# Kernel tuning notes

Measured on AMD Instinct MI355X. Metric: run time of the kernel, lower is better.

The kernel has to match this reference:

```python
import jax, jax.numpy as jnp
import numpy as np


def _sobel_mag(x_bchw):
    # per-channel Sobel gradient magnitude, then mean over channels -> [B,1,H,W]
    B, C, H, W = x_bchw.shape
    kx = jnp.array([[-1, 0, 1], [-2, 0, 2], [-1, 0, 1]], dtype=x_bchw.dtype).reshape(1, 1, 3, 3)
    ky = jnp.array([[-1, -2, -1], [0, 0, 0], [1, 2, 1]], dtype=x_bchw.dtype).reshape(1, 1, 3, 3)
    xf = x_bchw.reshape(B * C, 1, H, W)
    dn = ('NCHW', 'OIHW', 'NCHW')
    gx = jax.lax.conv_general_dilated(xf, kx, (1, 1), 'SAME', dimension_numbers=dn)
    gy = jax.lax.conv_general_dilated(xf, ky, (1, 1), 'SAME', dimension_numbers=dn)
    mag = jnp.sqrt(gx * gx + gy * gy + 1e-8).reshape(B, C, H, W)
    return mag.mean(axis=1, keepdims=True)


def _bi_wkv(w, u, k, v):
    # Bidirectional WKV (Vision-RWKV):
    # y_t = (sum_{i!=t} exp(k_i - (|t-i|-1)*w) v_i + exp(u+k_t) v_t)
    #     / (sum_{i!=t} exp(k_i - (|t-i|-1)*w)     + exp(u+k_t))
    # w,u: [C];  k,v: [B,T,C]. Numerically stable prefix scans in both directions.
    B, T, C = k.shape
    kt = jnp.transpose(k, (1, 0, 2))  # [T,B,C]
    vt = jnp.transpose(v, (1, 0, 2))

    def scan_dir(ks, vs):
        def step(carry, kv):
            a, b, pp = carry  # running num, den at log-offset pp (exclusive prefix)
            kk, vv = kv
            out = (a, b, pp)
            ww = pp - w  # decay one step
            p = jnp.maximum(ww, kk)
            e1 = jnp.exp(ww - p)
            e2 = jnp.exp(kk - p)
            return (e1 * a + e2 * vv, e1 * b + e2, p), out
        init = (jnp.zeros((B, C), k.dtype), jnp.zeros((B, C), k.dtype),
                jnp.full((B, C), -1e38, k.dtype))
        _, (a, b, pp) = jax.lax.scan(step, init, (ks, vs))
        return a, b, pp

    af, bf, pf = scan_dir(kt, vt)                       # contributions i < t
    ab, bb, pb = scan_dir(kt[::-1], vt[::-1])           # contributions i > t
    ab, bb, pb = ab[::-1], bb[::-1], pb[::-1]

    ps = u + kt                                         # self term exponent
    m = jnp.maximum(jnp.maximum(pf, pb), ps)
    ef = jnp.exp(pf - m)
    eb = jnp.exp(pb - m)
    es = jnp.exp(ps - m)
    num = af * ef + ab * eb + es * vt
    den = bf * ef + bb * eb + es
    return jnp.transpose(num / den, (1, 0, 2))  # [B,T,C]


def setup_inputs() -> dict:
    key = jax.random.key(0)
    ks = jax.random.split(key, 8)
    B, H, W, C = 8, 64, 64, 256
    T = H * W
    s = 1.0 / np.sqrt(C)
    return {
        'x': jax.random.normal(ks[0], (B, T, C), jnp.float32),
        'Wk': jax.random.normal(ks[1], (C, C), jnp.float32) * s,
        'Wv': jax.random.normal(ks[2], (C, C), jnp.float32) * s,
        'Wr': jax.random.normal(ks[3], (C, C), jnp.float32) * s,
        'Wo': jax.random.normal(ks[4], (C, C), jnp.float32) * s,
        'spatial_decay': jax.random.uniform(ks[5], (C,), jnp.float32, 0.5, 1.5),
        'spatial_first': jax.random.uniform(ks[6], (C,), jnp.float32, 0.5, 1.5),
        'H': H,
        'W': W,
    }


def reference(x, Wk, Wv, Wr, Wo, spatial_decay, spatial_first, H, W):
    B, T, C = x.shape
    k = x @ Wk.T
    v = x @ Wv.T
    r = x @ Wr.T
    sr = jax.nn.sigmoid(r)
    # edge gate
    x_hw = jnp.transpose(x, (0, 2, 1)).reshape(B, C, H, W)
    edge_g = jax.nn.sigmoid(_sobel_mag(x_hw)).reshape(B, 1, T)
    sr = sr + jnp.transpose(edge_g, (0, 2, 1))
    # bi-directional WKV with w,u scaled by 1/T (as in forward)
    xwkv = _bi_wkv(spatial_decay / T, spatial_first / T, k, v)
    return (sr * xwkv) @ Wo.T
```

## Files before the change

### kernel.cpp

```cpp
#include <hip/hip_runtime.h>
#include <hip/hip_bf16.h>

#define TB 8
#define TT 4096
#define TC 256
#define NC2 128
#define CL2 32

#define K2 512
#define BM 128
#define BN 128
#define BK 32

typedef _Float16 half8 __attribute__((ext_vector_type(8)));
typedef _Float16 half2v __attribute__((ext_vector_type(2)));
typedef float floatx4 __attribute__((ext_vector_type(4)));

#define GLDS16(g, l) __builtin_amdgcn_global_load_lds( \
    (const __attribute__((address_space(1))) void*)(g), \
    (__attribute__((address_space(3))) void*)(l), 16, 0, 0)

__global__ __launch_bounds__(256) void convert_x(
    const float* __restrict__ x, _Float16* __restrict__ X2, int n4)
{
    int t = blockIdx.x * 256 + threadIdx.x;
    if (t >= n4) return;
    float4 xv = ((const float4*)x)[t];
    half8 o;
    o[0] = (_Float16)xv.x; o[1] = (_Float16)(xv.x - (float)o[0]);
    o[2] = (_Float16)xv.y; o[3] = (_Float16)(xv.y - (float)o[2]);
    o[4] = (_Float16)xv.z; o[5] = (_Float16)(xv.z - (float)o[4]);
    o[6] = (_Float16)xv.w; o[7] = (_Float16)(xv.w - (float)o[6]);
    ((half8*)X2)[t] = o;
}

__global__ __launch_bounds__(256) void convert_w(
    const float* __restrict__ Wk, const float* __restrict__ Wv,
    const float* __restrict__ Wr, const float* __restrict__ Wo,
    _Float16* __restrict__ W2, _Float16* __restrict__ Wo2)
{
    int t = blockIdx.x * 256 + threadIdx.x;
    int wsel = t >> 16;
    int i = t & 65535;
    const float* src = (wsel == 0) ? Wk : (wsel == 1) ? Wv : (wsel == 2) ? Wr : Wo;
    _Float16* dst = (wsel < 3) ? (W2 + (size_t)wsel * TC * K2) : Wo2;
    _Float16 h = (_Float16)src[i];
    half2v p; p.x = h; p.y = h;
    *(half2v*)(dst + 2 * (size_t)i) = p;
}

__global__ __launch_bounds__(256) void gemm_f16(
    const _Float16* __restrict__ A2,
    const _Float16* __restrict__ W0, const _Float16* __restrict__ W1,
    const _Float16* __restrict__ W2p,
    float* __restrict__ C0, float* __restrict__ C1, float* __restrict__ C2,
    int sigmoid_mask)
{
    __shared__ _Float16 As[BM * BK];
    __shared__ _Float16 Bs[BN * BK];

    int by = blockIdx.y;
    int wsel = by >> 1;
    const _Float16* W = (wsel == 0) ? W0 : (wsel == 1) ? W1 : W2p;
    float* Cc         = (wsel == 0) ? C0 : (wsel == 1) ? C1 : C2;
    int col0 = (by & 1) * BN;
    int row0 = blockIdx.x * BM;
    int sig = (sigmoid_mask >> wsel) & 1;

    int tid = threadIdx.x;
    int lane = tid & 63;
    int wv = tid >> 6;
    int qm = (wv >> 1) * 64;
    int qn = (wv & 1) * 64;
    int mrow = lane & 15;
    int kgrp = (lane >> 4) * 8;

    const _Float16* Ag = A2 + (size_t)row0 * K2;
    const _Float16* Bg = W + (size_t)col0 * K2;

    floatx4 acc[4][4];
    #pragma unroll
    for (int i = 0; i < 4; i++)
        #pragma unroll
        for (int j = 0; j < 4; j++)
            acc[i][j] = (floatx4){0.f, 0.f, 0.f, 0.f};

    for (int kb = 0; kb < K2; kb += BK) {
        __syncthreads();
        #pragma unroll
        for (int r = 0; r < 2; r++) {
            int seg = r * 256 + tid;
            int row = seg >> 2;
            int ks = (seg & 3) * 8;
            GLDS16(Ag + (size_t)row * K2 + kb + ks, &As[seg * 8]);
            GLDS16(Bg + (size_t)row * K2 + kb + ks, &Bs[seg * 8]);
        }
        __syncthreads();
        half8 a[4], b[4];
        #pragma unroll
        for (int i = 0; i < 4; i++)
            a[i] = *(const half8*)&As[(qm + i * 16 + mrow) * BK + kgrp];
        #pragma unroll
        for (int j = 0; j < 4; j++)
            b[j] = *(const half8*)&Bs[(qn + j * 16 + mrow) * BK + kgrp];
        #pragma unroll
        for (int i = 0; i < 4; i++)
            #pragma unroll
            for (int j = 0; j < 4; j++)
                acc[i][j] = __builtin_amdgcn_mfma_f32_16x16x32_f16(
                    a[i], b[j], acc[i][j], 0, 0, 0);
    }

    int mr0 = (lane >> 4) * 4;
    int nc = lane & 15;
    #pragma unroll
    for (int i = 0; i < 4; i++) {
        #pragma unroll
        for (int r = 0; r < 4; r++) {
            int m = row0 + qm + i * 16 + mr0 + r;
            float* crow = Cc + (size_t)m * TC + col0 + qn;
            #pragma unroll
            for (int j = 0; j < 4; j++) {
                float vvv = acc[i][j][r];
                if (sig) vvv = 1.f / (1.f + __expf(-vvv));
                crow[j * 16 + nc] = vvv;
            }
        }
    }
}

__global__ __launch_bounds__(256) void sobel_edge(
    const float* __restrict__ x, float* __restrict__ edge)
{
    int t = blockIdx.x & (TT - 1);
    int b = blockIdx.x >> 12;
    int h = t >> 6, w = t & 63;
    int c = threadIdx.x;

    float n[3][3];
    #pragma unroll
    for (int dh = 0; dh < 3; dh++) {
        int hh = h + dh - 1;
        #pragma unroll
        for (int dw = 0; dw < 3; dw++) {
            int ww = w + dw - 1;
            float val = 0.f;
            if (hh >= 0 && hh < 64 && ww >= 0 && ww < 64)
                val = x[((size_t)(b * TT + (hh << 6) + ww)) * TC + c];
            n[dh][dw] = val;
        }
    }
    float gx = (n[0][2] - n[0][0]) + 2.f * (n[1][2] - n[1][0]) + (n[2][2] - n[2][0]);
    float gy = (n[2][0] + 2.f * n[2][1] + n[2][2]) - (n[0][0] + 2.f * n[0][1] + n[0][2]);
    float mag = sqrtf(gx * gx + gy * gy + 1e-8f);

    #pragma unroll
    for (int off = 32; off > 0; off >>= 1) mag += __shfl_down(mag, off, 64);
    __shared__ float part[4];
    if ((threadIdx.x & 63) == 0) part[threadIdx.x >> 6] = mag;
    __syncthreads();
    if (threadIdx.x == 0) {
        float s = part[0] + part[1] + part[2] + part[3];
        edge[blockIdx.x] = 1.f / (1.f + __expf(-s * (1.f / 256.f)));
    }
}

__global__ __launch_bounds__(256) void wkv_chunk_sums(
    const float* __restrict__ kp, const float* __restrict__ vp,
    const float* __restrict__ decay,
    float* __restrict__ SaF, float* __restrict__ SbF,
    float* __restrict__ RaB, float* __restrict__ RbB)
{
    int tid = blockIdx.x * 256 + threadIdx.x;
    int c = tid & 255;
    int j = (tid >> 8) & (NC2 - 1);
    int b = tid >> 15;
    float w = decay[c] * (1.f / (float)TT);
    float d = __expf(-w);
    size_t base = ((size_t)(b * TT + j * CL2)) * TC + c;
    float Sa = 0.f, Sb = 0.f, Ra = 0.f, Rb = 0.f, pw = 1.f;
    #pragma unroll
    for (int i = 0; i < CL2; i++) {
        float kk = kp[base + (size_t)i * TC];
        float vv = vp[base + (size_t)i * TC];
        float ek = __expf(kk);
        float ekv = ek * vv;
        Sa = fmaf(d, Sa, ekv);
        Sb = fmaf(d, Sb, ek);
        Ra = fmaf(pw, ekv, Ra);
        Rb = fmaf(pw, ek, Rb);
        pw *= d;
    }
    int idx = (b * NC2 + j) * TC + c;
    SaF[idx] = Sa; SbF[idx] = Sb; RaB[idx] = Ra; RbB[idx] = Rb;
}

__global__ __launch_bounds__(256) void wkv_carries(
    const float* __restrict__ SaF, const float* __restrict__ SbF,
    const float* __restrict__ RaB, const float* __restrict__ RbB,
    const float* __restrict__ decay,
    float* __restrict__ CfA, float* __restrict__ CfB,
    float* __restrict__ CbA, float* __restrict__ CbB)
{
    int tid = blockIdx.x * 256 + threadIdx.x;
    int c = tid & 255;
    int b = tid >> 8;
    float w = decay[c] * (1.f / (float)TT);
    float D = __expf(-(float)CL2 * w);
    float cfa = 0.f, cfb = 0.f;
    for (int j = 0; j < NC2; j++) {
        int idx = (b * NC2 + j) * TC + c;
        CfA[idx] = cfa; CfB[idx] = cfb;
        cfa = fmaf(D, cfa, SaF[idx]);
        cfb = fmaf(D, cfb, SbF[idx]);
    }
    float cba = 0.f, cbb = 0.f;
    for (int j = NC2 - 1; j >= 0; j--) {
        int idx = (b * NC2 + j) * TC + c;
        CbA[idx] = cba; CbB[idx] = cbb;
        cba = fmaf(D, cba, RaB[idx]);
        cbb = fmaf(D, cbb, RbB[idx]);
    }
}

__global__ __launch_bounds__(256) void wkv_combine(
    const float* __restrict__ kp, const float* __restrict__ vp,
    const float* __restrict__ srp, const float* __restrict__ edgep,
    const float* __restrict__ decay, const float* __restrict__ first,
    const float* __restrict__ CfA, const float* __restrict__ CfB,
    const float* __restrict__ CbA, const float* __restrict__ CbB,
    _Float16* __restrict__ Y2)
{
    int bid = blockIdx.x;
    int j = bid & (NC2 - 1);
    int b = bid >> 7;
    int c = threadIdx.x;

    float w = decay[c] * (1.f / (float)TT);
    float d = __expf(-w);
    float eu = __expf(first[c] * (1.f / (float)TT));
    int cidx = (b * NC2 + j) * TC + c;
    size_t base = ((size_t)(b * TT + j * CL2)) * TC + c;

    float abArr[CL2], bbArr[CL2];
    float ab = CbA[cidx], bb = CbB[cidx];
    #pragma unroll
    for (int i = CL2 - 1; i >= 0; i--) {
        float kk = kp[base + (size_t)i * TC];
        float vv = vp[base + (size_t)i * TC];
        float ek = __expf(kk);
        abArr[i] = ab; bbArr[i] = bb;
        ab = fmaf(d, ab, ek * vv);
        bb = fmaf(d, bb, ek);
    }
    float af = CfA[cidx], bf = CfB[cidx];
    #pragma unroll
    for (int i = 0; i < CL2; i++) {
        size_t idx = base + (size_t)i * TC;
        float kk = kp[idx];
        float vv = vp[idx];
        float srv = srp[idx];
        float ek = __expf(kk);
        float es = ek * eu;
        float num = af + abArr[i] + es * vv;
        float den = bf + bbArr[i] + es;
        float ev = edgep[b * TT + j * CL2 + i];
        float yv = (srv + ev) * (num / den);
        _Float16 yh = (_Float16)yv;
        _Float16 yl = (_Float16)(yv - (float)yh);
        half2v p; p.x = yh; p.y = yl;
        size_t m = (size_t)(b * TT + j * CL2 + i);
        *(half2v*)(Y2 + m * K2 + 2 * c) = p;
        af = fmaf(d, af, ek * vv);
        bf = fmaf(d, bf, ek);
    }
}

extern "C" void kernel_launch(void* const* d_in, const int* in_sizes, int n_in,
                              void* d_out, int out_size, void* d_ws, size_t ws_size,
                              hipStream_t stream)
{
    const float* x      = (const float*)d_in[0];
    const float* Wk     = (const float*)d_in[1];
    const float* Wv     = (const float*)d_in[2];
    const float* Wr     = (const float*)d_in[3];
    const float* Wo     = (const float*)d_in[4];
    const float* sdecay = (const float*)d_in[5];
    const float* sfirst = (const float*)d_in[6];
    float* out = (float*)d_out;

    char* ws = (char*)d_ws;
    size_t off = 0;
    const size_t MB32 = (size_t)TB * TT * TC * sizeof(float);
    const size_t XH   = (size_t)TB * TT * K2 * sizeof(_Float16);
    _Float16* X2  = (_Float16*)(ws + off); off += XH;
    float* kbuf  = (float*)(ws + off); off += MB32;
    float* vbuf  = (float*)(ws + off); off += MB32;
    float* srbuf = (float*)(ws + off); off += MB32;
    _Float16* W2  = (_Float16*)(ws + off); off += (size_t)3 * TC * K2 * sizeof(_Float16);
    _Float16* Wo2 = (_Float16*)(ws + off); off += (size_t)TC * K2 * sizeof(_Float16);
    float* edge  = (float*)(ws + off); off += (size_t)TB * TT * sizeof(float);
    const size_t CHB = (size_t)TB * NC2 * TC * sizeof(float);
    float* SaF = (float*)(ws + off); off += CHB;
    float* SbF = (float*)(ws + off); off += CHB;
    float* RaB = (float*)(ws + off); off += CHB;
    float* RbB = (float*)(ws + off); off += CHB;
    float* CfA = (float*)(ws + off); off += CHB;
    float* CfB = (float*)(ws + off); off += CHB;
    float* CbA = (float*)(ws + off); off += CHB;
    float* CbB = (float*)(ws + off); off += CHB;

    const int MBLK = (TB * TT) / BM;
    const int n4 = TB * TT * TC / 4;

    convert_w<<<(4 * TC * TC) / 256, 256, 0, stream>>>(Wk, Wv, Wr, Wo, W2, Wo2);
    convert_x<<<(n4 + 255) / 256, 256, 0, stream>>>(x, X2, n4);
    sobel_edge<<<TB * TT, 256, 0, stream>>>(x, edge);

    gemm_f16<<<dim3(MBLK, 6), 256, 0, stream>>>(
        X2, W2, W2 + (size_t)TC * K2, W2 + (size_t)2 * TC * K2,
        kbuf, vbuf, srbuf, 4);

    wkv_chunk_sums<<<(TB * NC2 * TC) / 256, 256, 0, stream>>>(
        kbuf, vbuf, sdecay, SaF, SbF, RaB, RbB);
    wkv_carries<<<(TB * TC) / 256, 256, 0, stream>>>(
        SaF, SbF, RaB, RbB, sdecay, CfA, CfB, CbA, CbB);
    wkv_combine<<<TB * NC2, 256, 0, stream>>>(
        kbuf, vbuf, srbuf, edge, sdecay, sfirst, CfA, CfB, CbA, CbB, X2);

    gemm_f16<<<dim3(MBLK, 2), 256, 0, stream>>>(
        X2, Wo2, Wo2, Wo2, out, out, out, 0);
}
```

Baseline: 247.6 us.

## Fuse x conversion into Sobel, store exp(k) as fp16, parallelize carries, widen GEMM K-tile

The x fp16 split-conversion is folded into the Sobel edge kernel, which removes one full pass over x. The k projection GEMM now applies exp in its epilogue and writes fp16 through a swizzled LDS tile, so later WKV kernels read half the bytes and skip their exp calls. The GEMM K tile grows to 64 with an XOR-swizzled LDS layout to reduce bank conflicts and barriers. The serial chunk-carry scan is replaced by a wavefront-parallel shuffle scan. Storing exp(k) in fp16 risks overflow or precision loss for large k.

Result: faster. 222.5 us (-10.1%).

```diff
diff --git a/kernel.cpp b/kernel.cpp
--- a/kernel.cpp
+++ b/kernel.cpp
@@ -10,7 +10,7 @@
 #define K2 512
 #define BM 128
 #define BN 128
-#define BK 32
+#define BK 64
 
 typedef _Float16 half8 __attribute__((ext_vector_type(8)));
 typedef _Float16 half2v __attribute__((ext_vector_type(2)));
@@ -20,18 +20,47 @@
     (const __attribute__((address_space(1))) void*)(g), \
     (__attribute__((address_space(3))) void*)(l), 16, 0, 0)
 
-__global__ __launch_bounds__(256) void convert_x(
-    const float* __restrict__ x, _Float16* __restrict__ X2, int n4)
-{
-    int t = blockIdx.x * 256 + threadIdx.x;
-    if (t >= n4) return;
-    float4 xv = ((const float4*)x)[t];
-    half8 o;
-    o[0] = (_Float16)xv.x; o[1] = (_Float16)(xv.x - (float)o[0]);
-    o[2] = (_Float16)xv.y; o[3] = (_Float16)(xv.y - (float)o[2]);
-    o[4] = (_Float16)xv.z; o[5] = (_Float16)(xv.z - (float)o[4]);
-    o[6] = (_Float16)xv.w; o[7] = (_Float16)(xv.w - (float)o[6]);
-    ((half8*)X2)[t] = o;
+__global__ __launch_bounds__(256) void sobconv(
+    const float* __restrict__ x, _Float16* __restrict__ X2,
+    float* __restrict__ edge)
+{
+    int t = blockIdx.x & (TT - 1);
+    int b = blockIdx.x >> 12;
+    int h = t >> 6, w = t & 63;
+    int c = threadIdx.x;
+
+    float n[3][3];
+    #pragma unroll
+    for (int dh = 0; dh < 3; dh++) {
+        int hh = h + dh - 1;
+        #pragma unroll
+        for (int dw = 0; dw < 3; dw++) {
+            int ww = w + dw - 1;
+            float val = 0.f;
+            if (hh >= 0 && hh < 64 && ww >= 0 && ww < 64)
+                val = x[((size_t)(b * TT + (hh << 6) + ww)) * TC + c];
+            n[dh][dw] = val;
+        }
+    }
+    float xc = n[1][1];
+    _Float16 hi = (_Float16)xc;
+    _Float16 lo = (_Float16)(xc - (float)hi);
+    half2v p; p.x = hi; p.y = lo;
+    *(half2v*)(X2 + ((size_t)(b * TT + t)) * K2 + 2 * c) = p;
+
+    float gx = (n[0][2] - n[0][0]) + 2.f * (n[1][2] - n[1][0]) + (n[2][2] - n[2][0]);
+    float gy = (n[2][0] + 2.f * n[2][1] + n[2][2]) - (n[0][0] + 2.f * n[0][1] + n[0][2]);
+    float mag = sqrtf(gx * gx + gy * gy + 1e-8f);
+
+    #pragma unroll
+    for (int off = 32; off > 0; off >>= 1) mag += __shfl_down(mag, off, 64);
+    __shared__ float part[4];
+    if ((threadIdx.x & 63) == 0) part[threadIdx.x >> 6] = mag;
+    __syncthreads();
+    if (threadIdx.x == 0) {
+        float s = part[0] + part[1] + part[2] + part[3];
+        edge[blockIdx.x] = 1.f / (1.f + __expf(-s * (1.f / 256.f)));
+    }
 }
 
 __global__ __launch_bounds__(256) void convert_w(
@@ -53,27 +82,26 @@
     const _Float16* __restrict__ A2,
     const _Float16* __restrict__ W0, const _Float16* __restrict__ W1,
     const _Float16* __restrict__ W2p,
-    float* __restrict__ C0, float* __restrict__ C1, float* __restrict__ C2,
-    int sigmoid_mask)
-{
-    __shared__ _Float16 As[BM * BK];
-    __shared__ _Float16 Bs[BN * BK];
+    void* __restrict__ C0, void* __restrict__ C1, void* __restrict__ C2,
+    int ops)
+{
+    __shared__ __align__(16) char smem[32768];
+    _Float16* As = (_Float16*)smem;
+    _Float16* Bs = (_Float16*)(smem + 16384);
 
     int by = blockIdx.y;
     int wsel = by >> 1;
     const _Float16* W = (wsel == 0) ? W0 : (wsel == 1) ? W1 : W2p;
-    float* Cc         = (wsel == 0) ? C0 : (wsel == 1) ? C1 : C2;
+    void* Cc          = (wsel == 0) ? C0 : (wsel == 1) ? C1 : C2;
     int col0 = (by & 1) * BN;
     int row0 = blockIdx.x * BM;
-    int sig = (sigmoid_mask >> wsel) & 1;
+    int op = (ops >> (2 * wsel)) & 3;
 
     int tid = threadIdx.x;
     int lane = tid & 63;
     int wv = tid >> 6;
     int qm = (wv >> 1) * 64;
     int qn = (wv & 1) * 64;
-    int mrow = lane & 15;
-    int kgrp = (lane >> 4) * 8;
 
     const _Float16* Ag = A2 + (size_t)row0 * K2;
     const _Float16* Bg = W + (size_t)col0 * K2;
@@ -88,85 +116,85 @@
     for (int kb = 0; kb < K2; kb += BK) {
         __syncthreads();
         #pragma unroll
-        for (int r = 0; r < 2; r++) {
-            int seg = r * 256 + tid;
-            int row = seg >> 2;
-            int ks = (seg & 3) * 8;
-            GLDS16(Ag + (size_t)row * K2 + kb + ks, &As[seg * 8]);
-            GLDS16(Bg + (size_t)row * K2 + kb + ks, &Bs[seg * 8]);
+        for (int i = 0; i < 4; i++) {
+            int seg = i * 256 + tid;
+            int row = seg >> 3;
+            int s = seg & 7;
+            int sg = s ^ (row & 7);
+            GLDS16(Ag + (size_t)row * K2 + kb + sg * 8, &As[seg * 8]);
+            GLDS16(Bg + (size_t)row * K2 + kb + sg * 8, &Bs[seg * 8]);
         }
         __syncthreads();
-        half8 a[4], b[4];
-        #pragma unroll
-        for (int i = 0; i < 4; i++)
-            a[i] = *(const half8*)&As[(qm + i * 16 + mrow) * BK + kgrp];
-        #pragma unroll
-        for (int j = 0; j < 4; j++)
-            b[j] = *(const half8*)&Bs[(qn + j * 16 + mrow) * BK + kgrp];
+        #pragma unroll
+        for (int kk = 0; kk < 2; kk++) {
+            int sl = kk * 4 + (lane >> 4);
+            half8 a[4], b[4];
+            #pragma unroll
+            for (int i = 0; i < 4; i++) {
+                int ra = qm + i * 16 + (lane & 15);
+                a[i] = *(const half8*)&As[ra * BK + ((sl ^ (ra & 7)) * 8)];
+                int rb = qn + i * 16 + (lane & 15);
+                b[i] = *(const half8*)&Bs[rb * BK + ((sl ^ (rb & 7)) * 8)];
+            }
+            #pragma unroll
+            for (int i = 0; i < 4; i++)
+                #pragma unroll
+                for (int j = 0; j < 4; j++)
+                    acc[i][j] = __builtin_amdgcn_mfma_f32_16x16x32_f16(
+                        a[i], b[j], acc[i][j], 0, 0, 0);
+        }
+    }
+
+    int mr0 = (lane >> 4) * 4;
+    int nc = lane & 15;
+    if (op == 2) {
+        __syncthreads();
+        ushort* tile = (ushort*)smem;
         #pragma unroll
         for (int i = 0; i < 4; i++)
             #pragma unroll
-            for (int j = 0; j < 4; j++)
-                acc[i][j] = __builtin_amdgcn_mfma_f32_16x16x32_f16(
-                    a[i], b[j], acc[i][j], 0, 0, 0);
-    }
-
-    int mr0 = (lane >> 4) * 4;
-    int nc = lane & 15;
-    #pragma unroll
-    for (int i = 0; i < 4; i++) {
-        #pragma unroll
-        for (int r = 0; r < 4; r++) {
-            int m = row0 + qm + i * 16 + mr0 + r;
-            float* crow = Cc + (size_t)m * TC + col0 + qn;
+            for (int r = 0; r < 4; r++) {
+                int ml = qm + i * 16 + mr0 + r;
+                #pragma unroll
+                for (int j = 0; j < 4; j++) {
+                    int nl = qn + j * 16 + nc;
+                    float vv = __expf(acc[i][j][r]);
+                    _Float16 hh = (_Float16)vv;
+                    tile[ml * 128 + (nl ^ (((ml >> 2) & 3) << 4))] = *(ushort*)&hh;
+                }
+            }
+        __syncthreads();
+        _Float16* Ch = (_Float16*)Cc;
+        #pragma unroll
+        for (int k = 0; k < 8; k++) {
+            int seg = k * 256 + tid;
+            int tr = seg >> 4;
+            int ts = seg & 15;
+            int ts2 = ts ^ (((tr >> 2) & 3) << 1);
+            float4 val = *(const float4*)&tile[tr * 128 + ts2 * 8];
+            ((float4*)(Ch + (size_t)(row0 + tr) * TC + col0))[ts] = val;
+        }
+    } else {
+        float* Cf = (float*)Cc;
+        #pragma unroll
+        for (int i = 0; i < 4; i++) {
             #pragma unroll
-            for (int j = 0; j < 4; j++) {
-                float vvv = acc[i][j][r];
-                if (sig) vvv = 1.f / (1.f + __expf(-vvv));
-                crow[j * 16 + nc] = vvv;
+            for (int r = 0; r < 4; r++) {
+                int m = row0 + qm + i * 16 + mr0 + r;
+                float* crow = Cf + (size_t)m * TC + col0 + qn;
+                #pragma unroll
+                for (int j = 0; j < 4; j++) {
+                    float vvv = acc[i][j][r];
+                    if (op == 1) vvv = 1.f / (1.f + __expf(-vvv));
+                    crow[j * 16 + nc] = vvv;
+                }
             }
         }
     }
 }
 
-__global__ __launch_bounds__(256) void sobel_edge(
-    const float* __restrict__ x, float* __restrict__ edge)
-{
-    int t = blockIdx.x & (TT - 1);
-    int b = blockIdx.x >> 12;
-    int h = t >> 6, w = t & 63;
-    int c = threadIdx.x;
-
-    float n[3][3];
-    #pragma unroll
-    for (int dh = 0; dh < 3; dh++) {
-        int hh = h + dh - 1;
-        #pragma unroll
-        for (int dw = 0; dw < 3; dw++) {
-            int ww = w + dw - 1;
-            float val = 0.f;
-            if (hh >= 0 && hh < 64 && ww >= 0 && ww < 64)
-                val = x[((size_t)(b * TT + (hh << 6) + ww)) * TC + c];
-            n[dh][dw] = val;
-        }
-    }
-    float gx = (n[0][2] - n[0][0]) + 2.f * (n[1][2] - n[1][0]) + (n[2][2] - n[2][0]);
-    float gy = (n[2][0] + 2.f * n[2][1] + n[2][2]) - (n[0][0] + 2.f * n[0][1] + n[0][2]);
-    float mag = sqrtf(gx * gx + gy * gy + 1e-8f);
-
-    #pragma unroll
-    for (int off = 32; off > 0; off >>= 1) mag += __shfl_down(mag, off, 64);
-    __shared__ float part[4];
-    if ((threadIdx.x & 63) == 0) part[threadIdx.x >> 6] = mag;
-    __syncthreads();
-    if (threadIdx.x == 0) {
-        float s = part[0] + part[1] + part[2] + part[3];
-        edge[blockIdx.x] = 1.f / (1.f + __expf(-s * (1.f / 256.f)));
-    }
-}
-
 __global__ __launch_bounds__(256) void wkv_chunk_sums(
-    const float* __restrict__ kp, const float* __restrict__ vp,
+    const _Float16* __restrict__ ekp, const float* __restrict__ vp,
     const float* __restrict__ decay,
     float* __restrict__ SaF, float* __restrict__ SbF,
     float* __restrict__ RaB, float* __restrict__ RbB)
@@ -181,9 +209,8 @@
     float Sa = 0.f, Sb = 0.f, Ra = 0.f, Rb = 0.f, pw = 1.f;
     #pragma unroll
     for (int i = 0; i < CL2; i++) {
-        float kk = kp[base + (size_t)i * TC];
+        float ek = (float)ekp[base + (size_t)i * TC];
         float vv = vp[base + (size_t)i * TC];
-        float ek = __expf(kk);
         float ekv = ek * vv;
         Sa = fmaf(d, Sa, ekv);
         Sb = fmaf(d, Sb, ek);
@@ -202,29 +229,54 @@
     float* __restrict__ CfA, float* __restrict__ CfB,
     float* __restrict__ CbA, float* __restrict__ CbB)
 {
-    int tid = blockIdx.x * 256 + threadIdx.x;
-    int c = tid & 255;
-    int b = tid >> 8;
+    int gw = (blockIdx.x * 256 + threadIdx.x) >> 6;
+    int lane = threadIdx.x & 63;
+    int c = gw & 255, b = gw >> 8;
     float w = decay[c] * (1.f / (float)TT);
     float D = __expf(-(float)CL2 * w);
-    float cfa = 0.f, cfb = 0.f;
-    for (int j = 0; j < NC2; j++) {
-        int idx = (b * NC2 + j) * TC + c;
-        CfA[idx] = cfa; CfB[idx] = cfb;
-        cfa = fmaf(D, cfa, SaF[idx]);
-        cfb = fmaf(D, cfb, SbF[idx]);
-    }
-    float cba = 0.f, cbb = 0.f;
-    for (int j = NC2 - 1; j >= 0; j--) {
-        int idx = (b * NC2 + j) * TC + c;
-        CbA[idx] = cba; CbB[idx] = cbb;
-        cba = fmaf(D, cba, RaB[idx]);
-        cbb = fmaf(D, cbb, RbB[idx]);
-    }
+    int base = b * NC2 * TC + c;
+    int j0 = 2 * lane, j1 = 2 * lane + 1;
+    int r0 = NC2 - 1 - j0, r1 = NC2 - 2 - j0;
+
+    float sa0 = SaF[base + j0 * TC], sa1 = SaF[base + j1 * TC];
+    float sb0 = SbF[base + j0 * TC], sb1 = SbF[base + j1 * TC];
+    float qa0 = RaB[base + r0 * TC], qa1 = RaB[base + r1 * TC];
+    float qb0 = RbB[base + r0 * TC], qb1 = RbB[base + r1 * TC];
+
+    float pa = fmaf(D, sa0, sa1), pb = fmaf(D, sb0, sb1);
+    float ra = fmaf(D, qa0, qa1), rb = fmaf(D, qb0, qb1);
+
+    float dp = D * D;
+    #pragma unroll
+    for (int off = 1; off < 64; off <<= 1) {
+        float ta = __shfl_up(pa, off, 64);
+        float tb = __shfl_up(pb, off, 64);
+        float ua = __shfl_up(ra, off, 64);
+        float ub = __shfl_up(rb, off, 64);
+        if (lane >= off) {
+            pa = fmaf(dp, ta, pa); pb = fmaf(dp, tb, pb);
+            ra = fmaf(dp, ua, ra); rb = fmaf(dp, ub, rb);
+        }
+        dp = dp * dp;
+    }
+    float ppa = __shfl_up(pa, 1, 64);
+    float ppb = __shfl_up(pb, 1, 64);
+    float pra = __shfl_up(ra, 1, 64);
+    float prb = __shfl_up(rb, 1, 64);
+    if (lane == 0) { ppa = 0.f; ppb = 0.f; pra = 0.f; prb = 0.f; }
+
+    CfA[base + j0 * TC] = ppa;
+    CfA[base + j1 * TC] = fmaf(D, ppa, sa0);
+    CfB[base + j0 * TC] = ppb;
+    CfB[base + j1 * TC] = fmaf(D, ppb, sb0);
+    CbA[base + r0 * TC] = pra;
+    CbA[base + r1 * TC] = fmaf(D, pra, qa0);
+    CbB[base + r0 * TC] = prb;
+    CbB[base + r1 * TC] = fmaf(D, prb, qb0);
 }
 
 __global__ __launch_bounds__(256) void wkv_combine(
-    const float* __restrict__ kp, const float* __restrict__ vp,
+    const _Float16* __restrict__ ekp, const float* __restrict__ vp,
     const float* __restrict__ srp, const float* __restrict__ edgep,
     const float* __restrict__ decay, const float* __restrict__ first,
     const float* __restrict__ CfA, const float* __restrict__ CfB,
@@ -246,9 +298,8 @@
     float ab = CbA[cidx], bb = CbB[cidx];
     #pragma unroll
     for (int i = CL2 - 1; i >= 0; i--) {
-        float kk = kp[base + (size_t)i * TC];
+        float ek = (float)ekp[base + (size_t)i * TC];
         float vv = vp[base + (size_t)i * TC];
-        float ek = __expf(kk);
         abArr[i] = ab; bbArr[i] = bb;
         ab = fmaf(d, ab, ek * vv);
         bb = fmaf(d, bb, ek);
@@ -257,10 +308,9 @@
     #pragma unroll
     for (int i = 0; i < CL2; i++) {
         size_t idx = base + (size_t)i * TC;
-        float kk = kp[idx];
+        float ek = (float)ekp[idx];
         float vv = vp[idx];
         float srv = srp[idx];
-        float ek = __expf(kk);
         float es = ek * eu;
         float num = af + abArr[i] + es * vv;
         float den = bf + bbArr[i] + es;
@@ -293,8 +343,8 @@
     size_t off = 0;
     const size_t MB32 = (size_t)TB * TT * TC * sizeof(float);
     const size_t XH   = (size_t)TB * TT * K2 * sizeof(_Float16);
-    _Float16* X2  = (_Float16*)(ws + off); off += XH;
-    float* kbuf  = (float*)(ws + off); off += MB32;
+    _Float16* X2   = (_Float16*)(ws + off); off += XH;
+    _Float16* ekh  = (_Float16*)(ws + off); off += MB32 / 2;
     float* vbuf  = (float*)(ws + off); off += MB32;
     float* srbuf = (float*)(ws + off); off += MB32;
     _Float16* W2  = (_Float16*)(ws + off); off += (size_t)3 * TC * K2 * sizeof(_Float16);
@@ -311,22 +361,21 @@
     float* CbB = (float*)(ws + off); off += CHB;
 
     const int MBLK = (TB * TT) / BM;
-    const int n4 = TB * TT * TC / 4;
 
     convert_w<<<(4 * TC * TC) / 256, 256, 0, stream>>>(Wk, Wv, Wr, Wo, W2, Wo2);
-    convert_x<<<(n4 + 255) / 256, 256, 0, stream>>>(x, X2, n4);
-    sobel_edge<<<TB * TT, 256, 0, stream>>>(x, edge);
-
+    sobconv<<<TB * TT, 256, 0, stream>>>(x, X2, edge);
+
+    int ops1 = (2 << 0) | (0 << 2) | (1 << 4);
     gemm_f16<<<dim3(MBLK, 6), 256, 0, stream>>>(
         X2, W2, W2 + (size_t)TC * K2, W2 + (size_t)2 * TC * K2,
-        kbuf, vbuf, srbuf, 4);
+        ekh, vbuf, srbuf, ops1);
 
     wkv_chunk_sums<<<(TB * NC2 * TC) / 256, 256, 0, stream>>>(
-        kbuf, vbuf, sdecay, SaF, SbF, RaB, RbB);
-    wkv_carries<<<(TB * TC) / 256, 256, 0, stream>>>(
+        ekh, vbuf, sdecay, SaF, SbF, RaB, RbB);
+    wkv_carries<<<(TB * TC * 64) / 256, 256, 0, stream>>>(
         SaF, SbF, RaB, RbB, sdecay, CfA, CfB, CbA, CbB);
     wkv_combine<<<TB * NC2, 256, 0, stream>>>(
-        kbuf, vbuf, srbuf, edge, sdecay, sfirst, CfA, CfB, CbA, CbB, X2);
+        ekh, vbuf, srbuf, edge, sdecay, sfirst, CfA, CfB, CbA, CbB, X2);
 
     gemm_f16<<<dim3(MBLK, 2), 256, 0, stream>>>(
         X2, Wo2, Wo2, Wo2, out, out, out, 0);
```
